# Kernel tuning notes

Measured on AMD Instinct MI355X. Metric: run time of the kernel, lower is better.

## Reference

```python
import jax, jax.numpy as jnp
import numpy as np

B, S, D, H = 2, 2048, 768, 12
HD = D // H  # head dim = 64

def setup_inputs() -> dict:
    key = jax.random.key(0)
    ks = jax.random.split(key, 9)
    s = 1.0 / np.sqrt(D)
    return {
        "x": jax.random.normal(ks[0], (B, S, D), dtype=jnp.float32),
        "Wq": jax.random.uniform(ks[1], (D, D), jnp.float32, -s, s),
        "bq": jax.random.uniform(ks[2], (D,), jnp.float32, -s, s),
        "Wk": jax.random.uniform(ks[3], (D, D), jnp.float32, -s, s),
        "bk": jax.random.uniform(ks[4], (D,), jnp.float32, -s, s),
        "Wv": jax.random.uniform(ks[5], (D, D), jnp.float32, -s, s),
        "bv": jax.random.uniform(ks[6], (D,), jnp.float32, -s, s),
        "Wo": jax.random.uniform(ks[7], (D, D), jnp.float32, -s, s),
        "bo": jax.random.uniform(ks[8], (D,), jnp.float32, -s, s),
    }

def reference(x, Wq, bq, Wk, bk, Wv, bv, Wo, bo):
    b, s, _ = x.shape
    # linear projections, split into heads: [b, h, s, hd]
    def proj(W, bias):
        y = x @ W + bias
        return y.reshape(b, s, H, HD).transpose(0, 2, 1, 3)
    q = proj(Wq, bq)
    k = proj(Wk, bk)
    v = proj(Wv, bv)
    scale = 1.0 / np.sqrt(HD).astype(np.float32)
    scores = jnp.einsum('bhqd,bhkd->bhqk', q, k) * scale
    attn = jax.nn.softmax(scores, axis=-1)
    out = jnp.einsum('bhqk,bhkd->bhqd', attn, v)
    out = out.transpose(0, 2, 1, 3).reshape(b, s, D)
    return out @ Wo + bo
```

## Files before the change

### kernel.cpp

```cpp
#include <hip/hip_runtime.h>
#include <math.h>

#define NH 12
#define SEQ 2048
#define DM 768
#define HD 64
#define NB 2
#define MT (NB * SEQ)
#define QSCL 0.18033688011112042591999058512524f

typedef short bf16x8 __attribute__((ext_vector_type(8)));
typedef float f32x16 __attribute__((ext_vector_type(16)));
typedef unsigned u32x2 __attribute__((ext_vector_type(2)));

__device__ __forceinline__ unsigned short bf16_rne(float x) {
    unsigned u = __float_as_uint(x);
    u += 0x7fffu + ((u >> 16) & 1u);
    return (unsigned short)(u >> 16);
}
__device__ __forceinline__ float bf16_tof(short h) {
    return __uint_as_float(((unsigned)(unsigned short)h) << 16);
}
__device__ __forceinline__ unsigned cvtpk(float lo, float hi) {
    unsigned r;
    asm("v_cvt_pk_bf16_f32 %0, %1, %2" : "=v"(r) : "v"(lo), "v"(hi));
    return r;
}

__device__ __forceinline__ void gl_lds16(const void* g, void* s) {
    __builtin_amdgcn_global_load_lds(
        (const __attribute__((address_space(1))) unsigned int*)g,
        (__attribute__((address_space(3))) unsigned int*)s, 16, 0, 0);
}

__device__ __forceinline__ f32x16 mfma32(bf16x8 a, bf16x8 b, f32x16 c) {
    return __builtin_amdgcn_mfma_f32_32x32x16_bf16(a, b, c, 0, 0, 0);
}

__device__ __forceinline__ bf16x8 gfrag(const char* base, int row, int physblk) {
    return *(const bf16x8*)(base + row * 64 + physblk * 16);
}
__device__ __forceinline__ bf16x8 afrag(const short* base, int row, int blk) {
    return *(const bf16x8*)(base + row * 64 + ((blk ^ (row & 7)) << 3));
}

__global__ __launch_bounds__(256)
void conv_all(const float* __restrict__ x,
              const float* __restrict__ Wq, const float* __restrict__ Wk,
              const float* __restrict__ Wv, const float* __restrict__ Wo,
              short* __restrict__ xg, short* __restrict__ wqkv,
              short* __restrict__ wo)
{
    int b = blockIdx.x;
    if (b < 1536) {
        const int idx = b * 256 + threadIdx.x;
        const int m = idx / 96, bk = idx % 96;
        const float* src = x + (size_t)m * DM + bk * 8;
        float4 v0 = *(const float4*)src;
        float4 v1 = *(const float4*)(src + 4);
        const float vv[8] = {v0.x, v0.y, v0.z, v0.w, v1.x, v1.y, v1.z, v1.w};
        union { short s[8]; int4 q; } hh;
#pragma unroll
        for (int j = 0; j < 8; j++) hh.s[j] = (short)bf16_rne(vv[j]);
        const int pb = (bk & ~3) | ((bk & 3) ^ ((m >> 1) & 3));
        *(int4*)(xg + (size_t)m * DM + pb * 8) = hh.q;
    } else {
        b -= 1536;
        const int z = b / 288;
        const float* __restrict__ W = (z == 0) ? Wq : (z == 1) ? Wk : (z == 2) ? Wv : Wo;
        short* __restrict__ wdst = (z == 3) ? wo : (wqkv + (size_t)z * 589824);
        const int idx = (b % 288) * 256 + threadIdx.x;
        const int n = idx % 768, bk = idx / 768;
        union { short s[8]; int4 q; } hh;
#pragma unroll
        for (int j = 0; j < 8; j++) hh.s[j] = (short)bf16_rne(W[(size_t)(bk * 8 + j) * DM + n]);
        const int pb = (bk & ~3) | ((bk & 3) ^ ((n >> 1) & 3));
        *(int4*)(wdst + (size_t)n * DM + pb * 8) = hh.q;
    }
}

template<bool SWAP>
__device__ __forceinline__ void qkv_loop(const char* pA, const char* pB,
                                         char* As, char* Bs,
                                         int t, f32x16* acc)
{
    const int w = t >> 6, l = t & 63;
    const int q32 = l & 31, half = l >> 5;
    const int sel = (q32 >> 1) & 3;
    const int arow  = 32 * (w & 1) + q32;
    const int brow0 = 64 * (w >> 1) + q32;
    char* const dA = As + w * 1024;
    char* const dB = Bs + w * 1024;

    auto stage = [&](int ki, int buf) {
        const size_t cb = (size_t)ki * 64;
        gl_lds16(pA + cb, dA + buf * 4096);
        gl_lds16(pB + cb, dB + buf * 8192);
        gl_lds16(pB + 64 * 1536 + cb, dB + buf * 8192 + 4096);
    };

    stage(0, 0);
    __syncthreads();

    for (int ki = 0; ki < 24; ki++) {
        const int cur = ki & 1;
        if (ki < 23) stage(ki + 1, cur ^ 1);
        const char* sA = As + cur * 4096;
        const char* sB = Bs + cur * 8192;
#pragma unroll
        for (int s = 0; s < 2; s++) {
            const int blk = (s * 2 + half) ^ sel;
            bf16x8 a  = gfrag(sA, arow, blk);
            bf16x8 b0 = gfrag(sB, brow0, blk);
            bf16x8 b1 = gfrag(sB, brow0 + 32, blk);
            if (SWAP) {
                acc[0] = mfma32(b0, a, acc[0]);
                acc[1] = mfma32(b1, a, acc[1]);
            } else {
                acc[0] = mfma32(a, b0, acc[0]);
                acc[1] = mfma32(a, b1, acc[1]);
            }
        }
        __syncthreads();
    }
}

__global__ __launch_bounds__(256)
void gemm_qkv(const short* __restrict__ xg, const short* __restrict__ wqkv,
              const float* __restrict__ bq, const float* __restrict__ bkv,
              const float* __restrict__ bv,
              short* __restrict__ qg, short* __restrict__ kg, short* __restrict__ vg)
{
    const int z = blockIdx.z;
    const short* __restrict__ Bw = wqkv + (size_t)z * 589824;
    const float* __restrict__ bias = (z == 0) ? bq : (z == 1) ? bkv : bv;

    __shared__ char As[8192], Bs[16384];
    const int t = threadIdx.x, w = t >> 6, l = t & 63;
    const int m0 = blockIdx.y * 64, n0 = blockIdx.x * 128;
    const int q32 = l & 31, half = l >> 5;

    const char* pA = (const char*)xg + (size_t)(m0 + (t >> 2)) * 1536 + (t & 3) * 16;
    const char* pB = (const char*)Bw + (size_t)(n0 + (t >> 2)) * 1536 + (t & 3) * 16;

    f32x16 acc[2];
#pragma unroll
    for (int i = 0; i < 2; i++)
#pragma unroll
        for (int r = 0; r < 16; r++) acc[i][r] = 0.f;

    if (z == 2) {
        qkv_loop<false>(pA, pB, As, Bs, t, acc);
        const int nbase = n0 + 64 * (w >> 1);
        const int h = nbase >> 6;
        const int mbase = m0 + 32 * (w & 1) + 4 * half;
        const int bb = mbase >> 11;
#pragma unroll
        for (int nt = 0; nt < 2; nt++) {
            const int hd = 32 * nt + q32;
            const float bia = bias[nbase + hd];
            short* vrow = vg + ((size_t)(bb * NH + h) * HD + hd) * SEQ;
#pragma unroll
            for (int g = 0; g < 4; g++) {
                const int ss0 = (mbase & 2047) + 8 * g;
                union { unsigned short u[4]; uint2 q; } pk;
#pragma unroll
                for (int j = 0; j < 4; j++)
                    pk.u[j] = bf16_rne(acc[nt][4 * g + j] + bia);
                const int blk = ss0 >> 3;
                const int phys = (blk & ~7) | ((blk & 7) ^ (hd & 7));
                *(uint2*)(vrow + phys * 8 + (ss0 & 7)) = pk.q;
            }
        }
    } else {
        qkv_loop<true>(pA, pB, As, Bs, t, acc);
        short* dst = (z == 0) ? qg : kg;
        const float scl = (z == 0) ? QSCL : 1.0f;
        const int mcol = m0 + 32 * (w & 1) + q32;
        const int bb = mcol >> 11, ss = mcol & 2047;
        const int h = (n0 + 64 * (w >> 1)) >> 6;
        short* drow = dst + ((size_t)(bb * NH + h) * SEQ + ss) * HD;
#pragma unroll
        for (int nt = 0; nt < 2; nt++)
#pragma unroll
            for (int g = 0; g < 4; g++) {
                const int hd0 = 32 * nt + 8 * g + 4 * half;
                float4 b4 = *(const float4*)&bias[(h << 6) + hd0];
                const float bb4[4] = {b4.x, b4.y, b4.z, b4.w};
                union { unsigned short u[4]; uint2 q; } pk;
#pragma unroll
                for (int j = 0; j < 4; j++)
                    pk.u[j] = bf16_rne((acc[nt][4 * g + j] + bb4[j]) * scl);
                const int phys = (hd0 >> 3) ^ (ss & 7);
                *(uint2*)(drow + phys * 8 + (hd0 & 7)) = pk.q;
            }
    }
}

__global__ __launch_bounds__(256)
void attn_mfma(const short* __restrict__ qg, const short* __restrict__ kg,
               const short* __restrict__ vg,
               short* __restrict__ opart, float* __restrict__ lpart)
{
    __shared__ short Qs[8192];
    __shared__ short Ks[4096];
    __shared__ short Vt[4096];

    const int t = threadIdx.x, w = t >> 6, l = t & 63;
    const int f = (blockIdx.x & 7) * 96 + (blockIdx.x >> 3);
    const int q0 = (f & 15) * 128;
    const int bh = (f >> 4) % 24;
    const int ks = f / 384;
    const char* qp = (const char*)(qg + (size_t)bh * SEQ * HD);
    const char* kp = (const char*)(kg + (size_t)bh * SEQ * HD);
    const char* vp = (const char*)(vg + (size_t)bh * HD * SEQ);
    const int kbase = ks * 1024;

#pragma unroll
    for (int i = 0; i < 4; i++)
        gl_lds16(qp + (size_t)(q0 + w * 32 + i * 8) * 128 + l * 16,
                 (char*)Qs + (w * 32 + i * 8) * 128);
#pragma unroll
    for (int i = 0; i < 2; i++) {
        gl_lds16(kp + (size_t)(kbase + w * 16 + i * 8) * 128 + l * 16,
                 (char*)Ks + (w * 16 + i * 8) * 128);
        gl_lds16(vp + (size_t)(w * 16 + i * 8 + (l >> 3)) * 4096 + kbase * 2 + (l & 7) * 16,
                 (char*)Vt + (w * 16 + i * 8) * 128);
    }
    __syncthreads();

    const int half = l >> 5;
    const int q = l & 31;
    bf16x8 qf[4];
#pragma unroll
    for (int s = 0; s < 4; s++)
        qf[s] = afrag(Qs, w * 32 + q, half + s * 2);
    __syncthreads();

    f32x16 oacc[2], lacc;
#pragma unroll
    for (int nt = 0; nt < 2; nt++)
#pragma unroll
        for (int r = 0; r < 16; r++) oacc[nt][r] = 0.f;
#pragma unroll
    for (int r = 0; r < 16; r++) lacc[r] = 0.f;

    bf16x8 onesf;
#pragma unroll
    for (int j = 0; j < 8; j++) onesf[j] = (short)0x3F80;

    for (int kti = 0; kti < 16; kti++) {
        const int cur = kti & 1;
        if (kti < 15) {
            const int kb0 = kbase + (kti + 1) * 64;
            char* kd = cur ? (char*)Ks : (char*)Qs;
            char* vd = cur ? (char*)Vt : (char*)(Qs + 4096);
#pragma unroll
            for (int i = 0; i < 2; i++) {
                gl_lds16(kp + (size_t)(kb0 + w * 16 + i * 8) * 128 + l * 16,
                         kd + (w * 16 + i * 8) * 128);
                gl_lds16(vp + (size_t)(w * 16 + i * 8 + (l >> 3)) * 4096 + kb0 * 2 + (l & 7) * 16,
                         vd + (w * 16 + i * 8) * 128);
            }
        }
        const short* kc = cur ? Qs : Ks;
        const short* vc = cur ? Qs + 4096 : Vt;

        f32x16 sacc[2];
#pragma unroll
        for (int nt = 0; nt < 2; nt++)
#pragma unroll
            for (int r = 0; r < 16; r++) sacc[nt][r] = 0.f;
#pragma unroll
        for (int s = 0; s < 4; s++)
#pragma unroll
            for (int nt = 0; nt < 2; nt++) {
                bf16x8 kf = afrag(kc, nt * 32 + q, half + s * 2);
                sacc[nt] = mfma32(kf, qf[s], sacc[nt]);
            }

#pragma unroll
        for (int nt = 0; nt < 2; nt++)
#pragma unroll
            for (int r = 0; r < 16; r++) sacc[nt][r] = exp2f(sacc[nt][r]);

#pragma unroll
        for (int s = 0; s < 4; s++) {
            const int nt = s >> 1;
            const int rb = (s & 1) * 8;
            const unsigned p0 = cvtpk(sacc[nt][rb + 0], sacc[nt][rb + 1]);
            const unsigned p1 = cvtpk(sacc[nt][rb + 2], sacc[nt][rb + 3]);
            const unsigned p2 = cvtpk(sacc[nt][rb + 4], sacc[nt][rb + 5]);
            const unsigned p3 = cvtpk(sacc[nt][rb + 6], sacc[nt][rb + 7]);
            const u32x2 w02 = __builtin_amdgcn_permlane32_swap(p0, p2, false, false);
            const u32x2 w13 = __builtin_amdgcn_permlane32_swap(p1, p3, false, false);
            union { unsigned u[4]; bf16x8 v; } pf;
            pf.u[0] = w02[0];
            pf.u[1] = w13[0];
            pf.u[2] = w02[1];
            pf.u[3] = w13[1];
            lacc = mfma32(pf.v, onesf, lacc);
#pragma unroll
            for (int nt2 = 0; nt2 < 2; nt2++) {
                bf16x8 vf = afrag(vc, nt2 * 32 + q, half + s * 2);
                oacc[nt2] = mfma32(pf.v, vf, oacc[nt2]);
            }
        }
        __syncthreads();
    }

    const size_t base = (size_t)(ks * 24 + bh) * SEQ;
#pragma unroll
    for (int r = 0; r < 16; r++) {
        const int row = q0 + w * 32 + (r & 3) + 8 * (r >> 2) + 4 * half;
#pragma unroll
        for (int nt = 0; nt < 2; nt++)
            opart[(base + row) * 64 + nt * 32 + q] = (short)bf16_rne(oacc[nt][r]);
        if (q == 0) lpart[base + row] = lacc[r];
    }
}

__global__ __launch_bounds__(256)
void attn_reduce(const short* __restrict__ opart, const float* __restrict__ lpart,
                 short* __restrict__ ag)
{
    const int idx = blockIdx.x * 256 + threadIdx.x;
    const int cg = idx & 7, row = idx >> 3;
    const int bh = row >> 11, s = row & 2047;
    union { short s[8]; int4 q; } a, b, o;
    a.q = *(const int4*)(opart + ((size_t)bh * SEQ + s) * 64 + cg * 8);
    b.q = *(const int4*)(opart + ((size_t)(24 + bh) * SEQ + s) * 64 + cg * 8);
    const float inv = 1.0f / (lpart[(size_t)bh * SEQ + s] + lpart[(size_t)(24 + bh) * SEQ + s]);
#pragma unroll
    for (int j = 0; j < 8; j++)
        o.s[j] = (short)bf16_rne((bf16_tof(a.s[j]) + bf16_tof(b.s[j])) * inv);
    const int bb = bh / NH, h = bh % NH;
    const int m = bb * SEQ + s;
    const int blk = h * 8 + cg;
    const int phys = (blk & ~3) | ((blk & 3) ^ ((m >> 1) & 3));
    *(int4*)(ag + (size_t)m * DM + phys * 8) = o.q;
}

__global__ __launch_bounds__(256)
void gemm_out(const short* __restrict__ ag, const short* __restrict__ wt3,
              const float* __restrict__ bias, float* __restrict__ out)
{
    __shared__ char As[8192], Bs[8192];
    const int t = threadIdx.x, w = t >> 6, l = t & 63;
    const int m0 = blockIdx.y * 64, n0 = blockIdx.x * 64;
    const int q32 = l & 31, half = l >> 5;
    const int sel = (q32 >> 1) & 3;

    const char* pA = (const char*)ag  + (size_t)(m0 + (t >> 2)) * 1536 + (t & 3) * 16;
    const char* pB = (const char*)wt3 + (size_t)(n0 + (t >> 2)) * 1536 + (t & 3) * 16;
    char* const dA = As + w * 1024;
    char* const dB = Bs + w * 1024;

    const int arow = 32 * (w & 1) + q32;
    const int brow = 32 * (w >> 1) + q32;

    f32x16 acc;
#pragma unroll
    for (int r = 0; r < 16; r++) acc[r] = 0.f;

    auto stage = [&](int ki, int buf) {
        const size_t cb = (size_t)ki * 64;
        gl_lds16(pA + cb, dA + buf * 4096);
        gl_lds16(pB + cb, dB + buf * 4096);
    };

    stage(0, 0);
    __syncthreads();

    for (int ki = 0; ki < 24; ki++) {
        const int cur = ki & 1;
        if (ki < 23) stage(ki + 1, cur ^ 1);
        const char* sA = As + cur * 4096;
        const char* sB = Bs + cur * 4096;
#pragma unroll
        for (int s = 0; s < 2; s++) {
            const int blk = (s * 2 + half) ^ sel;
            acc = mfma32(gfrag(sB, brow, blk), gfrag(sA, arow, blk), acc);
        }
        __syncthreads();
    }

    const int mcol = m0 + 32 * (w & 1) + q32;
    const int nb0 = n0 + 32 * (w >> 1) + 4 * half;
#pragma unroll
    for (int g = 0; g < 4; g++) {
        const int ng = nb0 + 8 * g;
        float4 b4 = *(const float4*)&bias[ng];
        float4 o;
        o.x = acc[4 * g + 0] + b4.x;
        o.y = acc[4 * g + 1] + b4.y;
        o.z = acc[4 * g + 2] + b4.z;
        o.w = acc[4 * g + 3] + b4.w;
        *(float4*)&out[(size_t)mcol * DM + ng] = o;
    }
}

extern "C" void kernel_launch(void* const* d_in, const int* in_sizes, int n_in,
                              void* d_out, int out_size, void* d_ws, size_t ws_size,
                              hipStream_t stream)
{
    const float* x  = (const float*)d_in[0];
    const float* Wq = (const float*)d_in[1];
    const float* bq = (const float*)d_in[2];
    const float* Wk = (const float*)d_in[3];
    const float* bk = (const float*)d_in[4];
    const float* Wv = (const float*)d_in[5];
    const float* bv = (const float*)d_in[6];
    const float* Wo = (const float*)d_in[7];
    const float* bo = (const float*)d_in[8];
    float* out = (float*)d_out;

    const size_t BUF = (size_t)MT * DM;
    short* base  = (short*)d_ws;
    short* wo    = base;
    short* qg    = base + 589824;
    short* kg    = qg + BUF;
    short* vg    = kg + BUF;
    short* opart = vg + BUF;
    float* lpart = (float*)(opart + (size_t)2 * 24 * SEQ * HD);
    short* xg    = opart;
    short* wqkv  = xg + BUF;
    short* ag    = qg;

    conv_all<<<2688, 256, 0, stream>>>(x, Wq, Wk, Wv, Wo, xg, wqkv, wo);
    gemm_qkv<<<dim3(6, 64, 3), 256, 0, stream>>>(xg, wqkv, bq, bk, bv, qg, kg, vg);
    attn_mfma<<<768, 256, 0, stream>>>(qg, kg, vg, opart, lpart);
    attn_reduce<<<1536, 256, 0, stream>>>(opart, lpart, ag);
    gemm_out<<<dim3(12, 64), 256, 0, stream>>>(ag, wo, bo, out);
}
```

Before: 194.2 us.

## Triple-buffer attention K/V with software-pipelined QK, fuse split-K reduce into output GEMM

The attention kernel moves to a three-slot LDS ring for K/V tiles, prefetching two tiles ahead. It computes the next tile's QK^T scores before the current tile's PV MFMAs, so the exp/convert work overlaps with matrix ops. Separately, the attn_reduce kernel is removed and its split-K sum and normalization move into the A-operand load of gemm_out. This saves a kernel launch and a round trip through global memory for the intermediate activations. In exchange, gemm_out redoes the reduction per N-tile (12x redundant loads of opart and lpart), and the larger LDS footprint may lower occupancy.

```diff
diff --git a/kernel.cpp b/kernel.cpp
--- a/kernel.cpp
+++ b/kernel.cpp
@@ -202,9 +202,10 @@
                const short* __restrict__ vg,
                short* __restrict__ opart, float* __restrict__ lpart)
 {
-    __shared__ short Qs[8192];
-    __shared__ short Ks[4096];
-    __shared__ short Vt[4096];
+    __shared__ __align__(16) short lds[24576];
+    short* const sl0 = lds + 8192;
+    short* const sl1 = lds + 16384;
+    short* const sl2 = lds;
 
     const int t = threadIdx.x, w = t >> 6, l = t & 63;
     const int f = (blockIdx.x & 7) * 96 + (blockIdx.x >> 3);
@@ -216,25 +217,36 @@
     const char* vp = (const char*)(vg + (size_t)bh * HD * SEQ);
     const int kbase = ks * 1024;
 
+    auto slot = [&](int i) -> short* {
+        const int md = i % 3;
+        return md == 0 ? sl0 : md == 1 ? sl1 : sl2;
+    };
+    auto stage_kv = [&](int tile, short* dst) {
+        const int kb0 = kbase + tile * 64;
+#pragma unroll
+        for (int i = 0; i < 2; i++) {
+            gl_lds16(kp + (size_t)(kb0 + w * 16 + i * 8) * 128 + l * 16,
+                     (char*)dst + (w * 16 + i * 8) * 128);
+            gl_lds16(vp + (size_t)(w * 16 + i * 8 + (l >> 3)) * 4096 + kb0 * 2 + (l & 7) * 16,
+                     (char*)(dst + 4096) + (w * 16 + i * 8) * 128);
+        }
+    };
+
 #pragma unroll
     for (int i = 0; i < 4; i++)
         gl_lds16(qp + (size_t)(q0 + w * 32 + i * 8) * 128 + l * 16,
-                 (char*)Qs + (w * 32 + i * 8) * 128);
-#pragma unroll
-    for (int i = 0; i < 2; i++) {
-        gl_lds16(kp + (size_t)(kbase + w * 16 + i * 8) * 128 + l * 16,
-                 (char*)Ks + (w * 16 + i * 8) * 128);
-        gl_lds16(vp + (size_t)(w * 16 + i * 8 + (l >> 3)) * 4096 + kbase * 2 + (l & 7) * 16,
-                 (char*)Vt + (w * 16 + i * 8) * 128);
-    }
-    __syncthreads();
+                 (char*)lds + (w * 32 + i * 8) * 128);
+    stage_kv(0, sl0);
+    stage_kv(1, sl1);
+
+    asm volatile("s_waitcnt vmcnt(8)" ::: "memory");
 
     const int half = l >> 5;
     const int q = l & 31;
     bf16x8 qf[4];
 #pragma unroll
     for (int s = 0; s < 4; s++)
-        qf[s] = afrag(Qs, w * 32 + q, half + s * 2);
+        qf[s] = afrag(lds, w * 32 + q, half + s * 2);
     __syncthreads();
 
     f32x16 oacc[2], lacc;
@@ -249,41 +261,24 @@
 #pragma unroll
     for (int j = 0; j < 8; j++) onesf[j] = (short)0x3F80;
 
+    f32x16 sacc[2];
+#pragma unroll
+    for (int nt = 0; nt < 2; nt++)
+#pragma unroll
+        for (int r = 0; r < 16; r++) sacc[nt][r] = 0.f;
+#pragma unroll
+    for (int s = 0; s < 4; s++)
+#pragma unroll
+        for (int nt = 0; nt < 2; nt++)
+            sacc[nt] = mfma32(afrag(sl0, nt * 32 + q, half + s * 2), qf[s], sacc[nt]);
+
     for (int kti = 0; kti < 16; kti++) {
-        const int cur = kti & 1;
-        if (kti < 15) {
-            const int kb0 = kbase + (kti + 1) * 64;
-            char* kd = cur ? (char*)Ks : (char*)Qs;
-            char* vd = cur ? (char*)Vt : (char*)(Qs + 4096);
-#pragma unroll
-            for (int i = 0; i < 2; i++) {
-                gl_lds16(kp + (size_t)(kb0 + w * 16 + i * 8) * 128 + l * 16,
-                         kd + (w * 16 + i * 8) * 128);
-                gl_lds16(vp + (size_t)(w * 16 + i * 8 + (l >> 3)) * 4096 + kb0 * 2 + (l & 7) * 16,
-                         vd + (w * 16 + i * 8) * 128);
-            }
-        }
-        const short* kc = cur ? Qs : Ks;
-        const short* vc = cur ? Qs + 4096 : Vt;
-
-        f32x16 sacc[2];
 #pragma unroll
         for (int nt = 0; nt < 2; nt++)
 #pragma unroll
-            for (int r = 0; r < 16; r++) sacc[nt][r] = 0.f;
-#pragma unroll
-        for (int s = 0; s < 4; s++)
-#pragma unroll
-            for (int nt = 0; nt < 2; nt++) {
-                bf16x8 kf = afrag(kc, nt * 32 + q, half + s * 2);
-                sacc[nt] = mfma32(kf, qf[s], sacc[nt]);
-            }
-
-#pragma unroll
-        for (int nt = 0; nt < 2; nt++)
-#pragma unroll
             for (int r = 0; r < 16; r++) sacc[nt][r] = exp2f(sacc[nt][r]);
 
+        bf16x8 pfs[4];
 #pragma unroll
         for (int s = 0; s < 4; s++) {
             const int nt = s >> 1;
@@ -299,12 +294,31 @@
             pf.u[1] = w13[0];
             pf.u[2] = w02[1];
             pf.u[3] = w13[1];
-            lacc = mfma32(pf.v, onesf, lacc);
-#pragma unroll
-            for (int nt2 = 0; nt2 < 2; nt2++) {
-                bf16x8 vf = afrag(vc, nt2 * 32 + q, half + s * 2);
-                oacc[nt2] = mfma32(pf.v, vf, oacc[nt2]);
-            }
+            pfs[s] = pf.v;
+        }
+
+        if (kti < 14) stage_kv(kti + 2, slot(kti + 2));
+
+        if (kti < 15) {
+            const short* kc = slot(kti + 1);
+#pragma unroll
+            for (int nt = 0; nt < 2; nt++)
+#pragma unroll
+                for (int r = 0; r < 16; r++) sacc[nt][r] = 0.f;
+#pragma unroll
+            for (int s = 0; s < 4; s++)
+#pragma unroll
+                for (int nt = 0; nt < 2; nt++)
+                    sacc[nt] = mfma32(afrag(kc, nt * 32 + q, half + s * 2), qf[s], sacc[nt]);
+        }
+
+        const short* vc = slot(kti) + 4096;
+#pragma unroll
+        for (int s = 0; s < 4; s++) {
+            lacc = mfma32(pfs[s], onesf, lacc);
+#pragma unroll
+            for (int nt2 = 0; nt2 < 2; nt2++)
+                oacc[nt2] = mfma32(pfs[s], afrag(vc, nt2 * 32 + q, half + s * 2), oacc[nt2]);
         }
         __syncthreads();
     }
@@ -321,29 +335,9 @@
 }
 
 __global__ __launch_bounds__(256)
-void attn_reduce(const short* __restrict__ opart, const float* __restrict__ lpart,
-                 short* __restrict__ ag)
-{
-    const int idx = blockIdx.x * 256 + threadIdx.x;
-    const int cg = idx & 7, row = idx >> 3;
-    const int bh = row >> 11, s = row & 2047;
-    union { short s[8]; int4 q; } a, b, o;
-    a.q = *(const int4*)(opart + ((size_t)bh * SEQ + s) * 64 + cg * 8);
-    b.q = *(const int4*)(opart + ((size_t)(24 + bh) * SEQ + s) * 64 + cg * 8);
-    const float inv = 1.0f / (lpart[(size_t)bh * SEQ + s] + lpart[(size_t)(24 + bh) * SEQ + s]);
-#pragma unroll
-    for (int j = 0; j < 8; j++)
-        o.s[j] = (short)bf16_rne((bf16_tof(a.s[j]) + bf16_tof(b.s[j])) * inv);
-    const int bb = bh / NH, h = bh % NH;
-    const int m = bb * SEQ + s;
-    const int blk = h * 8 + cg;
-    const int phys = (blk & ~3) | ((blk & 3) ^ ((m >> 1) & 3));
-    *(int4*)(ag + (size_t)m * DM + phys * 8) = o.q;
-}
-
-__global__ __launch_bounds__(256)
-void gemm_out(const short* __restrict__ ag, const short* __restrict__ wt3,
-              const float* __restrict__ bias, float* __restrict__ out)
+void gemm_out(const short* __restrict__ opart, const float* __restrict__ lpart,
+              const short* __restrict__ wt3, const float* __restrict__ bias,
+              float* __restrict__ out)
 {
     __shared__ char As[8192], Bs[8192];
     const int t = threadIdx.x, w = t >> 6, l = t & 63;
@@ -351,9 +345,12 @@
     const int q32 = l & 31, half = l >> 5;
     const int sel = (q32 >> 1) & 3;
 
-    const char* pA = (const char*)ag  + (size_t)(m0 + (t >> 2)) * 1536 + (t & 3) * 16;
+    const int r = t >> 2, c4 = t & 3;
+    const int m = m0 + r;
+    const int b = m >> 11, s = m & 2047;
+    char* const dAw = As + r * 64 + (c4 ^ ((r >> 1) & 3)) * 16;
+
     const char* pB = (const char*)wt3 + (size_t)(n0 + (t >> 2)) * 1536 + (t & 3) * 16;
-    char* const dA = As + w * 1024;
     char* const dB = Bs + w * 1024;
 
     const int arow = 32 * (w & 1) + q32;
@@ -361,27 +358,45 @@
 
     f32x16 acc;
 #pragma unroll
-    for (int r = 0; r < 16; r++) acc[r] = 0.f;
-
-    auto stage = [&](int ki, int buf) {
-        const size_t cb = (size_t)ki * 64;
-        gl_lds16(pA + cb, dA + buf * 4096);
-        gl_lds16(pB + cb, dB + buf * 4096);
-    };
-
-    stage(0, 0);
+    for (int rr = 0; rr < 16; rr++) acc[rr] = 0.f;
+
+    union i4u { short sh[8]; int4 q; };
+    i4u o0, o1;
+    float inv;
+
+    auto loadA = [&](int ki) {
+        const int h = ki >> 1;
+        const size_t lrow = (size_t)(b * NH + h) * SEQ + s;
+        const size_t obase = lrow * 64 + (ki & 1) * 32 + c4 * 8;
+        o0.q = *(const int4*)(opart + obase);
+        o1.q = *(const int4*)(opart + obase + (size_t)24 * SEQ * 64);
+        inv = 1.0f / (lpart[lrow] + lpart[lrow + (size_t)24 * SEQ]);
+    };
+    auto writeA = [&](int buf) {
+        i4u oa;
+#pragma unroll
+        for (int j = 0; j < 8; j++)
+            oa.sh[j] = (short)bf16_rne((bf16_tof(o0.sh[j]) + bf16_tof(o1.sh[j])) * inv);
+        *(int4*)(dAw + buf * 4096) = oa.q;
+    };
+    auto stageB = [&](int ki, int buf) {
+        gl_lds16(pB + (size_t)ki * 64, dB + buf * 4096);
+    };
+
+    loadA(0); writeA(0); stageB(0, 0);
     __syncthreads();
 
     for (int ki = 0; ki < 24; ki++) {
         const int cur = ki & 1;
-        if (ki < 23) stage(ki + 1, cur ^ 1);
+        if (ki < 23) { stageB(ki + 1, cur ^ 1); loadA(ki + 1); }
         const char* sA = As + cur * 4096;
         const char* sB = Bs + cur * 4096;
 #pragma unroll
-        for (int s = 0; s < 2; s++) {
-            const int blk = (s * 2 + half) ^ sel;
+        for (int ss = 0; ss < 2; ss++) {
+            const int blk = (ss * 2 + half) ^ sel;
             acc = mfma32(gfrag(sB, brow, blk), gfrag(sA, arow, blk), acc);
         }
+        if (ki < 23) writeA(cur ^ 1);
         __syncthreads();
     }
 
@@ -425,11 +440,9 @@
     float* lpart = (float*)(opart + (size_t)2 * 24 * SEQ * HD);
     short* xg    = opart;
     short* wqkv  = xg + BUF;
-    short* ag    = qg;
 
     conv_all<<<2688, 256, 0, stream>>>(x, Wq, Wk, Wv, Wo, xg, wqkv, wo);
     gemm_qkv<<<dim3(6, 64, 3), 256, 0, stream>>>(xg, wqkv, bq, bk, bv, qg, kg, vg);
     attn_mfma<<<768, 256, 0, stream>>>(qg, kg, vg, opart, lpart);
-    attn_reduce<<<1536, 256, 0, stream>>>(opart, lpart, ag);
-    gemm_out<<<dim3(12, 64), 256, 0, stream>>>(ag, wo, bo, out);
-}
+    gemm_out<<<dim3(12, 64), 256, 0, stream>>>(opart, lpart, wo, bo, out);
+}
```

Result: no change. 196.3 us (+1.1%).
